# Performance work log

Measured on AMD Instinct MI355X. Metric: run time of the kernel, lower is better.

The kernel has to match this reference:

```python
import jax, jax.numpy as jnp
import numpy as np

N_SAMPLES = 256   # n_samples from __init__
N_THIN = 10       # N from __init__
N_WORDS = 4096


def setup_inputs() -> dict:
    key = jax.random.key(0)
    k1, k2, k3 = jax.random.split(key, 3)
    # scale potentials so per-step weight deltas stay in a sane exp() range
    bigram = jax.random.normal(k1, (N_WORDS, N_WORDS), dtype=jnp.float32)
    start = jax.random.normal(k2, (N_WORDS,), dtype=jnp.float32)
    end = jax.random.normal(k3, (N_WORDS,), dtype=jnp.float32)
    return {"n_words": N_WORDS, "bigram": bigram, "start": start, "end": end}


def _mh_chain(bigram, start, end, n_words, chain_size, rng):
    # chain[0] = identity permutation (random_start=False)
    perm0 = jnp.arange(n_words, dtype=jnp.int32)
    w0 = bigram[perm0[:-1], perm0[1:]].sum() + start[perm0[0]] + end[perm0[-1]]

    def step(carry, k):
        perm, w_last = carry
        k_pos, k_cat, k_u = jax.random.split(k, 3)
        # pick a token to move, remove it -> perm2 of length n_words-1
        pos = jax.random.randint(k_pos, (), 0, n_words)
        to_move = perm[pos]
        j = jnp.arange(n_words - 1)
        perm2 = perm[j + (j >= pos).astype(j.dtype)]
        # insertion logits over n_words slots (self._probs, unnormalized log p)
        logits = jnp.zeros((n_words,), dtype=bigram.dtype)
        logits = logits.at[0].add(start[to_move]).at[-1].add(end[to_move])
        logits = logits.at[1:].add(bigram[perm2, to_move])   # left-neighbor term
        logits = logits.at[:-1].add(bigram[to_move, perm2])  # right-neighbor term
        p = jax.nn.softmax(logits)
        new_pos = jax.random.categorical(k_cat, logits)
        # insert to_move at new_pos
        jj = jnp.arange(n_words)
        shifted = perm2[jnp.clip(jj - (jj > new_pos).astype(jj.dtype), 0, n_words - 2)]
        sample = jnp.where(jj == new_pos, to_move, shifted).astype(perm.dtype)
        # new chain weight
        new_w = bigram[sample[:-1], sample[1:]].sum() + start[sample[0]] + end[sample[-1]]
        # MH accept ratio; removing to_move from sample recovers perm2, so the
        # reverse insertion distribution equals p -> ratio p[new_pos]/p[pos]
        acc = jnp.minimum(1.0, jnp.exp(new_w - w_last) * p[new_pos] / p[pos])
        accept = acc > jax.random.uniform(k_u, ())
        perm_next = jnp.where(accept, sample, perm)
        w_next = jnp.where(accept, new_w, w_last)
        return (perm_next, w_next), perm_next

    keys = jax.random.split(rng, chain_size - 1)
    _, perms = jax.lax.scan(step, (perm0, w0), keys)
    chain = jnp.concatenate([perm0[None, :], perms], axis=0)  # [chain_size, n_words]
    sel = jnp.arange(0, chain_size, N_THIN) + (N_THIN - 1)    # thin: every N-th state
    return chain[sel]


def reference(n_words, bigram, start, end):
    chain_size = N_SAMPLES * N_THIN
    rng = jax.random.key(42)
    return _mh_chain(bigram, start, end, n_words, chain_size, rng)
```

## Files before the change

kernel.cpp:

```cpp
#include <hip/hip_runtime.h>
#include <stdint.h>


#define NW 4096
#define NSTEPS 2559
#define NTHREADS 1024
#define NWAVES 16

typedef unsigned long long u64;
typedef uint32_t u32;
typedef unsigned short u16;

__device__ __forceinline__ u32 rotl32(u32 v, u32 r) { return (v << r) | (v >> (32u - r)); }

__device__ __forceinline__ void tf2x32(u32 k0, u32 k1, u32 x0, u32 x1, u32* o0, u32* o1) {
  u32 ks2 = k0 ^ k1 ^ 0x1BD11BDAu;
  x0 += k0; x1 += k1;
#define TFR(r0, r1, r2, r3)                      \
  x0 += x1; x1 = rotl32(x1, r0); x1 ^= x0;       \
  x0 += x1; x1 = rotl32(x1, r1); x1 ^= x0;       \
  x0 += x1; x1 = rotl32(x1, r2); x1 ^= x0;       \
  x0 += x1; x1 = rotl32(x1, r3); x1 ^= x0;
  TFR(13, 15, 26, 6)  x0 += k1;  x1 += ks2 + 1u;
  TFR(17, 29, 16, 24) x0 += ks2; x1 += k0 + 2u;
  TFR(13, 15, 26, 6)  x0 += k0;  x1 += k1 + 3u;
  TFR(17, 29, 16, 24) x0 += k1;  x1 += ks2 + 4u;
  TFR(13, 15, 26, 6)  x0 += ks2; x1 += k0 + 5u;
#undef TFR
  *o0 = x0; *o1 = x1;
}

__device__ __forceinline__ float unif01(u32 bits) {
  return __uint_as_float((bits >> 9) | 0x3f800000u) - 1.0f;
}

__device__ __forceinline__ u32 fkey(float f) {
  u32 b = __float_as_uint(f);
  return b ^ ((b >> 31) ? 0xFFFFFFFFu : 0x80000000u);
}


template <int CTRL>
__device__ __forceinline__ u32 dpp32(u32 v) {
  return (u32)__builtin_amdgcn_update_dpp(0, (int)v, CTRL, 0xF, 0xF, true);
}

template <int CTRL>
__device__ __forceinline__ void dppmax64(u32& hi, u32& lo) {
  u32 h2 = dpp32<CTRL>(hi);
  u32 l2 = dpp32<CTRL>(lo);
  bool g = (h2 > hi) || (h2 == hi && l2 > lo);
  hi = g ? h2 : hi;
  lo = g ? l2 : lo;
}

__device__ __forceinline__ u64 wave_max_u64(u64 key) {
  u32 lo = (u32)key, hi = (u32)(key >> 32);
  dppmax64<0x111>(hi, lo); dppmax64<0x112>(hi, lo);
  dppmax64<0x114>(hi, lo); dppmax64<0x118>(hi, lo);
  dppmax64<0x142>(hi, lo); dppmax64<0x143>(hi, lo);
  return ((u64)hi << 32) | lo;
}

__device__ __forceinline__ u64 bfly16_max_u64(u64 key) {
  u32 lo = (u32)key, hi = (u32)(key >> 32);
  dppmax64<0xB1>(hi, lo); dppmax64<0x4E>(hi, lo);
  dppmax64<0x141>(hi, lo); dppmax64<0x140>(hi, lo);
  return ((u64)hi << 32) | lo;
}


#define TT 32
__global__ void transpose_k(const float* __restrict__ in, float* __restrict__ out) {
  __shared__ float tile[TT][TT + 1];
  int x = blockIdx.x * TT + threadIdx.x;
  int y = blockIdx.y * TT + threadIdx.y;
  for (int j = 0; j < TT; j += 8) tile[threadIdx.y + j][threadIdx.x] = in[(u64)(y + j) * NW + x];
  __syncthreads();
  x = blockIdx.y * TT + threadIdx.x;
  y = blockIdx.x * TT + threadIdx.y;
  for (int j = 0; j < TT; j += 8) out[(u64)(y + j) * NW + x] = tile[threadIdx.x][threadIdx.y + j];
}

__global__ void gumbel_k(float* __restrict__ gumb) {
  long long idx = (long long)blockIdx.x * blockDim.x + threadIdx.x;
  if (idx >= (long long)NSTEPS * NW) return;
  int t = (int)(idx >> 12);
  int p = (int)(idx & (NW - 1));
  int i = (p >> 2) | ((p & 3) << 10);
  u32 kt0, kt1, kc0, kc1, ba, bb;
  tf2x32(0u, 42u, 0u, (u32)t, &kt0, &kt1);
  tf2x32(kt0, kt1, 0u, 1u, &kc0, &kc1);
  tf2x32(kc0, kc1, 0u, (u32)i, &ba, &bb);
  float u = unif01(ba ^ bb);
  if (u == 0.0f) u = 1.17549435e-38f;
  float t1 = (float)log((double)u);
  float t2 = (float)log((double)(-t1));
  gumb[idx] = -t2;
}

__global__ void posu_k(int* __restrict__ posArr, float* __restrict__ uArr) {
  int t = blockIdx.x * blockDim.x + threadIdx.x;
  if (t >= NSTEPS) return;
  u32 kt0, kt1, kp0, kp1, ku0, ku1, k2a, k2b, ra, rb, ua, ub;
  tf2x32(0u, 42u, 0u, (u32)t, &kt0, &kt1);
  tf2x32(kt0, kt1, 0u, 0u, &kp0, &kp1);
  tf2x32(kt0, kt1, 0u, 2u, &ku0, &ku1);
  tf2x32(kp0, kp1, 0u, 1u, &k2a, &k2b);
  tf2x32(k2a, k2b, 0u, 0u, &ra, &rb);
  posArr[t] = (int)((ra ^ rb) & (u32)(NW - 1));
  tf2x32(ku0, ku1, 0u, 0u, &ua, &ub);
  uArr[t] = unif01(ua ^ ub);
}


#define SAMPLE_AT(idx)                                                        \
  ((idx) < np ? (int)s_perm[(idx) + ((idx) >= pos)]                           \
              : ((idx) == np ? tm                                             \
                             : (int)s_perm[((idx)-1) + (((idx)-1) >= pos)]))

__global__ __launch_bounds__(NTHREADS)
void mcmc_fast10(const float* __restrict__ bigram,
                 const float* __restrict__ bigT,
                 const float* __restrict__ gumb,
                 const int* __restrict__ posArr,
                 const float* __restrict__ uArr,
                 const float* __restrict__ startv,
                 const float* __restrict__ endv,
                 int* __restrict__ out) {
  __shared__ u16    s_perm[NW];
  __shared__ float  s_rowB[NW];
  __shared__ float  s_rowT[NW];
  __shared__ u64    s_redu[NWAVES];
  __shared__ float  s_stm, s_etm, s_lpos;
  __shared__ int    s_accs;

  const int tid = threadIdx.x;
  const int lane = tid & 63;
  const int wid = tid >> 6;

  for (int i = tid; i < NW; i += NTHREADS) s_perm[i] = (u16)i;

  int pos = posArr[0];
  int tm = pos;
  {
    float4 rb4 = ((const float4*)(bigram + (u64)tm * NW))[tid];
    float4 rt4 = ((const float4*)(bigT + (u64)tm * NW))[tid];
    ((float4*)s_rowB)[tid] = rb4;
    ((float4*)s_rowT)[tid] = rt4;
  }
  if (tid == 0) { s_stm = startv[tm]; s_etm = endv[tm]; }

  float u_cur = uArr[0];
  float start_cur = startv[0];
  float end_cur = endv[NW - 1];
  float brg = 0.0f;
  if (pos >= 1 && pos <= NW - 2) brg = bigram[(u64)(pos - 1) * NW + (pos + 1)];

  float4 g4 = ((const float4*)gumb)[tid];
  __syncthreads();

  for (int t = 0; t < NSTEPS; ++t) {
    const float gg[4] = {g4.x, g4.y, g4.z, g4.w};
    int pos_nxt; float u_nxt;
    {
      int tn = (t + 1 < NSTEPS) ? (t + 1) : (NSTEPS - 1);
      g4 = ((const float4*)(gumb + ((u64)tn << 12)))[tid];
      pos_nxt = posArr[tn];
      u_nxt = uArr[tn];
    }
    u64 best = 0;
#pragma unroll
    for (int k = 0; k < 4; ++k) {
      int i = tid + k * NTHREADS;
      float li;
      if (i == 0) {
        int r = s_perm[(0 >= pos) ? 1 : 0];
        li = s_stm + s_rowB[r];
      } else if (i == NW - 1) {
        int l = s_perm[((NW - 2) >= pos) ? (NW - 1) : (NW - 2)];
        li = s_etm + s_rowT[l];
      } else {
        int l = s_perm[(i - 1) + ((i - 1) >= pos)];
        int r = s_perm[i + (i >= pos)];
        li = s_rowT[l] + s_rowB[r];
      }
      if (i == pos) s_lpos = li;
      float sv = gg[k] + li;
      u64 key = ((u64)fkey(sv) << 32) | (u32)(NW - 1 - i);
      if (key > best) best = key;
    }
    best = wave_max_u64(best);
    if (lane == 63) s_redu[wid] = best;
    __syncthreads();

    int np;
    {
      u64 bb = bfly16_max_u64(s_redu[lane & 15]);
      np = NW - 1 - (int)(bb & 0xFFFFFFFFu);
    }
    const int tmR = (int)s_perm[pos_nxt];
    const int tmA = SAMPLE_AT(pos_nxt);
    u16 stash[4];
#pragma unroll
    for (int k = 0; k < 4; ++k) {
      int j = tid + k * NTHREADS;
      stash[k] = (j < np) ? s_perm[j + (j >= pos)]
                          : ((j == np) ? (u16)tm : s_perm[(j - 1) + ((j - 1) >= pos)]);
    }
    int plA = 0, prA = 0, plR = 0, prR = 0;
    const bool ibn = (pos_nxt >= 1 && pos_nxt <= NW - 2);
    if (wid == 0) {
      int ls_i = (np >= 1) ? ((np - 1) + ((np - 1) >= pos)) : 0;
      int rs_i = (np <= NW - 2) ? (np + (np >= pos)) : 0;
      const int l_s = (int)s_perm[ls_i];
      const int r_s = (int)s_perm[rs_i];
      float splitv = bigram[(u64)l_s * NW + r_s];
      int s0 = (np > 0) ? (int)s_perm[(0 >= pos) ? 1 : 0] : tm;
      int sl = (np < NW - 1) ? (int)s_perm[(NW - 2) + ((NW - 2) >= pos)] : tm;
      float sv0 = startv[s0];
      float ev1 = endv[sl];
      float remL = 0.0f, remR = 0.0f;
      if (pos > 0)      remL = s_rowT[s_perm[pos - 1]];
      if (pos < NW - 1) remR = s_rowB[s_perm[pos + 1]];
      float vnpm1 = (np >= 1)      ? s_rowT[l_s] : 0.0f;
      float vnp   = (np <= NW - 2) ? s_rowB[r_s] : 0.0f;
      if (ibn) {
        plR = (int)s_perm[pos_nxt - 1]; prR = (int)s_perm[pos_nxt + 1];
        plA = SAMPLE_AT(pos_nxt - 1);   prA = SAMPLE_AT(pos_nxt + 1);
      }
      float stm_r = s_stm, etm_r = s_etm;
      float lposv = s_lpos;
      double delta = 0.0;
      if (pos > 0)               delta -= (double)remL;
      if (pos < NW - 1)          delta -= (double)remR;
      if (pos > 0 && pos < NW-1) delta += (double)brg;
      if (np > 0)                delta += (double)vnpm1;
      if (np < NW - 1)           delta += (double)vnp;
      if (np > 0 && np < NW - 1) delta -= (double)splitv;
      delta += ((double)sv0 - (double)start_cur) + ((double)ev1 - (double)end_cur);
      float lnp = (np == 0) ? (stm_r + vnp)
                : ((np == NW - 1) ? (etm_r + vnpm1) : (vnpm1 + vnp));
      double ed = delta + ((double)lnp - (double)lposv);
      float a = fminf(1.0f, (float)exp(ed));
      int acc = (a > u_cur) ? 1 : 0;
      if (lane == 0) s_accs = acc;
      if (acc) { start_cur = sv0; end_cur = ev1; }
    }
    __syncthreads();

    const int acc = s_accs;
    const int tm_next = acc ? tmA : tmR;
    const float4 rb4 = ((const float4*)(bigram + (u64)tm_next * NW))[tid];
    const float4 rt4 = ((const float4*)(bigT + (u64)tm_next * NW))[tid];
    if (wid == 0) {
      float stmN = startv[tm_next];
      float etmN = endv[tm_next];
      brg = 0.0f;
      if (ibn) {
        int pl = acc ? plA : plR;
        int pr = acc ? prA : prR;
        brg = bigram[(u64)pl * NW + pr];
      }
      if (lane == 0) { s_stm = stmN; s_etm = etmN; }
    }
    if (acc) {
#pragma unroll
      for (int k = 0; k < 4; ++k) {
        int j = tid + k * NTHREADS;
        s_perm[j] = stash[k];
      }
    }
    ((float4*)s_rowB)[tid] = rb4;
    ((float4*)s_rowT)[tid] = rt4;
    tm = tm_next;
    pos = pos_nxt;
    u_cur = u_nxt;
    __syncthreads();

    if ((t % 10) == 8) {
      int row = (t - 8) / 10;
      ushort4 p4 = ((const ushort4*)s_perm)[tid];
      int4 o4;
      o4.x = (int)p4.x; o4.y = (int)p4.y; o4.z = (int)p4.z; o4.w = (int)p4.w;
      ((int4*)(out + (u64)row * NW))[tid] = o4;
    }
  }
}


__global__ __launch_bounds__(NTHREADS)
void mcmc_kernel(const float* __restrict__ bigram,
                 const float* __restrict__ startv,
                 const float* __restrict__ endv,
                 int* __restrict__ out) {
  __shared__ int    s_perm[NW];
  __shared__ float  s_logit[NW];
  __shared__ float  s_gath[NW];
  __shared__ float  s_redf[NWAVES];
  __shared__ u64    s_redu[NWAVES];
  __shared__ double s_redd[NWAVES];
  __shared__ float  s_m, s_Z, s_w;
  __shared__ int    s_pos, s_tm, s_np, s_acc;
  __shared__ u32    s_kcat0, s_kcat1, s_ku0, s_ku1;

  const int tid = threadIdx.x;
  const int lane = tid & 63;
  const int wid = tid >> 6;

  for (int i = tid; i < NW; i += NTHREADS) s_perm[i] = i;
  for (int j = tid; j < NW - 1; j += NTHREADS) s_gath[j] = bigram[(u64)j * NW + (j + 1)];
  __syncthreads();
  if (tid == 0) {
    float S = 0.0f;
    for (int j = 0; j < NW - 1; ++j) S += s_gath[j];
    S = S + startv[0];
    S = S + endv[NW - 1];
    s_w = S;
  }
  __syncthreads();

  for (int t = 0; t < NSTEPS; ++t) {
    if (tid == 0) {
      u32 kt0, kt1;
      tf2x32(0u, 42u, 0u, (u32)t, &kt0, &kt1);
      u32 kp0, kp1, kc0, kc1, ku0, ku1;
      tf2x32(kt0, kt1, 0u, 0u, &kp0, &kp1);
      tf2x32(kt0, kt1, 0u, 1u, &kc0, &kc1);
      tf2x32(kt0, kt1, 0u, 2u, &ku0, &ku1);
      u32 k2a, k2b, ra, rb;
      tf2x32(kp0, kp1, 0u, 1u, &k2a, &k2b);
      tf2x32(k2a, k2b, 0u, 0u, &ra, &rb);
      int pos = (int)((ra ^ rb) & (u32)(NW - 1));
      s_pos = pos;
      s_tm = s_perm[pos];
      s_kcat0 = kc0; s_kcat1 = kc1; s_ku0 = ku0; s_ku1 = ku1;
    }
    __syncthreads();
    const int pos = s_pos, tm = s_tm;

    float lmax = -3.402823466e+38f;
    for (int i = tid; i < NW; i += NTHREADS) {
      float li;
      if (i == 0) {
        int r = s_perm[(0 >= pos) ? 1 : 0];
        li = startv[tm] + bigram[(u64)tm * NW + r];
      } else if (i == NW - 1) {
        int l = s_perm[((NW - 2) >= pos) ? (NW - 1) : (NW - 2)];
        li = endv[tm] + bigram[(u64)l * NW + tm];
      } else {
        int l = s_perm[((i - 1) >= pos) ? i : (i - 1)];
        int r = s_perm[(i >= pos) ? (i + 1) : i];
        li = bigram[(u64)l * NW + tm] + bigram[(u64)tm * NW + r];
      }
      s_logit[i] = li;
      lmax = fmaxf(lmax, li);
    }
    for (int o = 32; o > 0; o >>= 1) lmax = fmaxf(lmax, __shfl_down(lmax, o, 64));
    if (lane == 0) s_redf[wid] = lmax;
    __syncthreads();
    if (tid == 0) {
      float m = s_redf[0];
      for (int w = 1; w < NWAVES; ++w) m = fmaxf(m, s_redf[w]);
      s_m = m;
    }
    __syncthreads();
    const float m = s_m;

    double zacc = 0.0;
    u64 best = 0;
    const u32 kc0 = s_kcat0, kc1 = s_kcat1;
    for (int i = tid; i < NW; i += NTHREADS) {
      float li = s_logit[i];
      float ex = (float)exp((double)(li - m));
      zacc += (double)ex;
      u32 ba, bb;
      tf2x32(kc0, kc1, 0u, (u32)i, &ba, &bb);
      float u = unif01(ba ^ bb);
      if (u == 0.0f) u = 1.17549435e-38f;
      float t1 = (float)log((double)u);
      float t2 = (float)log((double)(-t1));
      float g = -t2;
      float sv = g + li;
      u64 key = ((u64)fkey(sv) << 32) | (u32)(NW - 1 - i);
      if (key > best) best = key;
    }
    for (int o = 32; o > 0; o >>= 1) {
      u64 w = __shfl_down(best, o, 64);
      if (w > best) best = w;
      zacc += __shfl_down(zacc, o, 64);
    }
    if (lane == 0) { s_redu[wid] = best; s_redd[wid] = zacc; }
    __syncthreads();
    if (tid == 0) {
      u64 b = s_redu[0]; double z = s_redd[0];
      for (int w = 1; w < NWAVES; ++w) {
        if (s_redu[w] > b) b = s_redu[w];
        z += s_redd[w];
      }
      s_np = NW - 1 - (int)(b & 0xFFFFFFFFu);
      s_Z = (float)z;
    }
    __syncthreads();
    const int np = s_np;

    for (int j = tid; j < NW - 1; j += NTHREADS) {
      int a = (j < np) ? s_perm[j + (j >= pos)]
                       : ((j == np) ? tm : s_perm[(j - 1) + ((j - 1) >= pos)]);
      int j1 = j + 1;
      int b = (j1 < np) ? s_perm[j1 + (j1 >= pos)]
                        : ((j1 == np) ? tm : s_perm[(j1 - 1) + ((j1 - 1) >= pos)]);
      s_gath[j] = bigram[(u64)a * NW + b];
    }
    __syncthreads();

    if (tid == 0) {
      float S = 0.0f;
      for (int j = 0; j < NW - 1; ++j) S += s_gath[j];
      int s0 = (0 < np) ? s_perm[(0 >= pos) ? 1 : 0] : tm;
      int sl = ((NW - 1) == np) ? tm : s_perm[(NW - 2) + ((NW - 2) >= pos)];
      S = S + startv[s0];
      S = S + endv[sl];
      float dw = S - s_w;
      float e1 = (float)exp((double)dw);
      float en = (float)exp((double)(s_logit[np] - m));
      float eo = (float)exp((double)(s_logit[pos] - m));
      float pn = en / s_Z;
      float po = eo / s_Z;
      float acc = e1 * pn;
      acc = acc / po;
      acc = fminf(1.0f, acc);
      u32 ua, ub;
      tf2x32(s_ku0, s_ku1, 0u, 0u, &ua, &ub);
      float u = unif01(ua ^ ub);
      int accept = (acc > u) ? 1 : 0;
      s_acc = accept;
      if (accept) s_w = S;
    }
    __syncthreads();

    int stash[4];
    if (s_acc) {
      for (int k = 0; k < 4; ++k) {
        int i = tid + k * NTHREADS;
        stash[k] = (i < np) ? s_perm[i + (i >= pos)]
                            : ((i == np) ? tm : s_perm[(i - 1) + ((i - 1) >= pos)]);
      }
    }
    __syncthreads();
    if (s_acc) {
      for (int k = 0; k < 4; ++k) {
        int i = tid + k * NTHREADS;
        s_perm[i] = stash[k];
      }
    }
    __syncthreads();

    if (((t + 1) % 10) == 9) {
      int row = (t - 8) / 10;
      for (int i = tid; i < NW; i += NTHREADS) out[(u64)row * NW + i] = s_perm[i];
    }
    __syncthreads();
  }
}

extern "C" void kernel_launch(void* const* d_in, const int* in_sizes, int n_in,
                              void* d_out, int out_size, void* d_ws, size_t ws_size,
                              hipStream_t stream) {
  const float* bigram = (const float*)d_in[1];
  const float* startv = (const float*)d_in[2];
  const float* endv   = (const float*)d_in[3];
  int* out = (int*)d_out;

  const size_t needT = (size_t)NW * NW * sizeof(float);
  const size_t needG = (size_t)NSTEPS * NW * sizeof(float);
  const size_t needP = (size_t)NSTEPS * (sizeof(int) + sizeof(float));

  if (ws_size >= needT + needG + needP) {
    float* bigT = (float*)d_ws;
    float* gumb = (float*)((char*)d_ws + needT);
    int* posArr = (int*)((char*)d_ws + needT + needG);
    float* uArr = (float*)((char*)d_ws + needT + needG + (size_t)NSTEPS * sizeof(int));
    hipLaunchKernelGGL(transpose_k, dim3(NW / TT, NW / TT), dim3(TT, 8), 0, stream,
                       bigram, bigT);
    long long ng = (long long)NSTEPS * NW;
    hipLaunchKernelGGL(gumbel_k, dim3((unsigned)((ng + 255) / 256)), dim3(256), 0, stream,
                       gumb);
    hipLaunchKernelGGL(posu_k, dim3((NSTEPS + 255) / 256), dim3(256), 0, stream,
                       posArr, uArr);
    hipLaunchKernelGGL(mcmc_fast10, dim3(1), dim3(NTHREADS), 0, stream,
                       bigram, bigT, gumb, posArr, uArr, startv, endv, out);
  } else {
    hipLaunchKernelGGL(mcmc_kernel, dim3(1), dim3(NTHREADS), 0, stream,
                       bigram, startv, endv, out);
  }
}
```

Measured before the change: 7.521 ms.

## Interleave bigram rows in LDS and assign contiguous slots per thread with DPP neighbors

Each thread now owns four consecutive insertion slots instead of four strided ones. It reads its perm entries with a single ushort4 load and gets neighbouring entries via DPP lane shifts. The two per-step bigram rows are interleaved into a single float2 array so that left and right terms come from one LDS read, and the gumbel layout is changed to match. The accept exponential also switches from double exp to float expf. This cuts LDS traffic and index arithmetic in the serial per-step loop, but float2 gathers may add bank conflicts, and expf could shift the accept decision in rare borderline cases.

```diff
diff --git a/kernel.cpp b/kernel.cpp
--- a/kernel.cpp
+++ b/kernel.cpp
@@ -86,8 +86,7 @@
   long long idx = (long long)blockIdx.x * blockDim.x + threadIdx.x;
   if (idx >= (long long)NSTEPS * NW) return;
   int t = (int)(idx >> 12);
-  int p = (int)(idx & (NW - 1));
-  int i = (p >> 2) | ((p & 3) << 10);
+  int i = (int)(idx & (NW - 1));
   u32 kt0, kt1, kc0, kc1, ba, bb;
   tf2x32(0u, 42u, 0u, (u32)t, &kt0, &kt1);
   tf2x32(kt0, kt1, 0u, 1u, &kc0, &kc1);
@@ -120,7 +119,7 @@
                              : (int)s_perm[((idx)-1) + (((idx)-1) >= pos)]))
 
 __global__ __launch_bounds__(NTHREADS)
-void mcmc_fast10(const float* __restrict__ bigram,
+void mcmc_fast11(const float* __restrict__ bigram,
                  const float* __restrict__ bigT,
                  const float* __restrict__ gumb,
                  const int* __restrict__ posArr,
@@ -129,8 +128,7 @@
                  const float* __restrict__ endv,
                  int* __restrict__ out) {
   __shared__ u16    s_perm[NW];
-  __shared__ float  s_rowB[NW];
-  __shared__ float  s_rowT[NW];
+  __shared__ float2 s_rows[NW];
   __shared__ u64    s_redu[NWAVES];
   __shared__ float  s_stm, s_etm, s_lpos;
   __shared__ int    s_accs;
@@ -138,6 +136,7 @@
   const int tid = threadIdx.x;
   const int lane = tid & 63;
   const int wid = tid >> 6;
+  const int j0 = tid * 4;
 
   for (int i = tid; i < NW; i += NTHREADS) s_perm[i] = (u16)i;
 
@@ -146,8 +145,8 @@
   {
     float4 rb4 = ((const float4*)(bigram + (u64)tm * NW))[tid];
     float4 rt4 = ((const float4*)(bigT + (u64)tm * NW))[tid];
-    ((float4*)s_rowB)[tid] = rb4;
-    ((float4*)s_rowT)[tid] = rt4;
+    ((float4*)(&s_rows[j0]))[0] = make_float4(rt4.x, rb4.x, rt4.y, rb4.y);
+    ((float4*)(&s_rows[j0]))[1] = make_float4(rt4.z, rb4.z, rt4.w, rb4.w);
   }
   if (tid == 0) { s_stm = startv[tm]; s_etm = endv[tm]; }
 
@@ -169,26 +168,47 @@
       pos_nxt = posArr[tn];
       u_nxt = uArr[tn];
     }
-    u64 best = 0;
-#pragma unroll
-    for (int k = 0; k < 4; ++k) {
-      int i = tid + k * NTHREADS;
-      float li;
-      if (i == 0) {
-        int r = s_perm[(0 >= pos) ? 1 : 0];
-        li = s_stm + s_rowB[r];
-      } else if (i == NW - 1) {
-        int l = s_perm[((NW - 2) >= pos) ? (NW - 1) : (NW - 2)];
-        li = s_etm + s_rowT[l];
-      } else {
-        int l = s_perm[(i - 1) + ((i - 1) >= pos)];
-        int r = s_perm[i + (i >= pos)];
-        li = s_rowT[l] + s_rowB[r];
-      }
-      if (i == pos) s_lpos = li;
-      float sv = gg[k] + li;
-      u64 key = ((u64)fkey(sv) << 32) | (u32)(NW - 1 - i);
-      if (key > best) best = key;
+    ushort4 pq = ((const ushort4*)s_perm)[tid];
+    const int p0i = pq.x, p1i = pq.y, p2i = pq.z, p3i = pq.w;
+    int pm1, pp4;
+    {
+      u32 lo = (u32)pq.x | ((u32)pq.y << 16);
+      u32 hi = (u32)pq.z | ((u32)pq.w << 16);
+      pm1 = (int)(dpp32<0x138>(hi) >> 16);
+      pp4 = (int)(dpp32<0x130>(lo) & 0xFFFFu);
+      if (lane == 0)  pm1 = (tid > 0) ? (int)s_perm[j0 - 1] : 0;
+      if (lane == 63) pp4 = (tid < NTHREADS - 1) ? (int)s_perm[j0 + 4] : 0;
+    }
+    const int w0 = (j0     >= pos) ? p1i : p0i;
+    const int w1 = (j0 + 1 >= pos) ? p2i : p1i;
+    const int w2 = (j0 + 2 >= pos) ? p3i : p2i;
+    const int w3 = (j0 + 3 >= pos) ? pp4 : p3i;
+    const int wprev = ((j0 - 1) >= pos) ? p0i : pm1;
+    const float2 f0 = s_rows[w0];
+    const float2 f1 = s_rows[w1];
+    const float2 f2 = s_rows[w2];
+    const float2 f3 = s_rows[w3];
+    float tprev = __uint_as_float(dpp32<0x138>(__float_as_uint(f3.x)));
+    if (lane == 0 && tid > 0) tprev = s_rows[wprev].x;
+    float li0 = tprev + f0.y;
+    float li1 = f0.x + f1.y;
+    float li2 = f1.x + f2.y;
+    float li3 = f2.x + f3.y;
+    if (tid == 0)            li0 = s_stm + f0.y;
+    if (tid == NTHREADS - 1) li3 = s_etm + f2.x;
+    if ((pos >> 2) == tid) {
+      int k = pos & 3;
+      s_lpos = (k == 0) ? li0 : ((k == 1) ? li1 : ((k == 2) ? li2 : li3));
+    }
+    u64 best;
+    {
+      u64 b0 = ((u64)fkey(gg[0] + li0) << 32) | (u32)(NW - 1 - j0);
+      u64 b1 = ((u64)fkey(gg[1] + li1) << 32) | (u32)(NW - 2 - j0);
+      u64 b2 = ((u64)fkey(gg[2] + li2) << 32) | (u32)(NW - 3 - j0);
+      u64 b3 = ((u64)fkey(gg[3] + li3) << 32) | (u32)(NW - 4 - j0);
+      best = b0 > b1 ? b0 : b1;
+      u64 b23 = b2 > b3 ? b2 : b3;
+      if (b23 > best) best = b23;
     }
     best = wave_max_u64(best);
     if (lane == 63) s_redu[wid] = best;
@@ -201,13 +221,11 @@
     }
     const int tmR = (int)s_perm[pos_nxt];
     const int tmA = SAMPLE_AT(pos_nxt);
-    u16 stash[4];
-#pragma unroll
-    for (int k = 0; k < 4; ++k) {
-      int j = tid + k * NTHREADS;
-      stash[k] = (j < np) ? s_perm[j + (j >= pos)]
-                          : ((j == np) ? (u16)tm : s_perm[(j - 1) + ((j - 1) >= pos)]);
-    }
+    ushort4 st;
+    st.x = (j0     < np) ? (u16)w0 : ((j0     == np) ? (u16)tm : (u16)wprev);
+    st.y = (j0 + 1 < np) ? (u16)w1 : ((j0 + 1 == np) ? (u16)tm : (u16)w0);
+    st.z = (j0 + 2 < np) ? (u16)w2 : ((j0 + 2 == np) ? (u16)tm : (u16)w1);
+    st.w = (j0 + 3 < np) ? (u16)w3 : ((j0 + 3 == np) ? (u16)tm : (u16)w2);
     int plA = 0, prA = 0, plR = 0, prR = 0;
     const bool ibn = (pos_nxt >= 1 && pos_nxt <= NW - 2);
     if (wid == 0) {
@@ -221,10 +239,10 @@
       float sv0 = startv[s0];
       float ev1 = endv[sl];
       float remL = 0.0f, remR = 0.0f;
-      if (pos > 0)      remL = s_rowT[s_perm[pos - 1]];
-      if (pos < NW - 1) remR = s_rowB[s_perm[pos + 1]];
-      float vnpm1 = (np >= 1)      ? s_rowT[l_s] : 0.0f;
-      float vnp   = (np <= NW - 2) ? s_rowB[r_s] : 0.0f;
+      if (pos > 0)      remL = s_rows[s_perm[pos - 1]].x;
+      if (pos < NW - 1) remR = s_rows[s_perm[pos + 1]].y;
+      float vnpm1 = (np >= 1)      ? s_rows[l_s].x : 0.0f;
+      float vnp   = (np <= NW - 2) ? s_rows[r_s].y : 0.0f;
       if (ibn) {
         plR = (int)s_perm[pos_nxt - 1]; prR = (int)s_perm[pos_nxt + 1];
         plA = SAMPLE_AT(pos_nxt - 1);   prA = SAMPLE_AT(pos_nxt + 1);
@@ -232,17 +250,17 @@
       float stm_r = s_stm, etm_r = s_etm;
       float lposv = s_lpos;
       double delta = 0.0;
-      if (pos > 0)               delta -= (double)remL;
-      if (pos < NW - 1)          delta -= (double)remR;
-      if (pos > 0 && pos < NW-1) delta += (double)brg;
-      if (np > 0)                delta += (double)vnpm1;
-      if (np < NW - 1)           delta += (double)vnp;
-      if (np > 0 && np < NW - 1) delta -= (double)splitv;
+      if (pos > 0)                 delta -= (double)remL;
+      if (pos < NW - 1)            delta -= (double)remR;
+      if (pos > 0 && pos < NW - 1) delta += (double)brg;
+      if (np > 0)                  delta += (double)vnpm1;
+      if (np < NW - 1)             delta += (double)vnp;
+      if (np > 0 && np < NW - 1)   delta -= (double)splitv;
       delta += ((double)sv0 - (double)start_cur) + ((double)ev1 - (double)end_cur);
       float lnp = (np == 0) ? (stm_r + vnp)
                 : ((np == NW - 1) ? (etm_r + vnpm1) : (vnpm1 + vnp));
       double ed = delta + ((double)lnp - (double)lposv);
-      float a = fminf(1.0f, (float)exp(ed));
+      float a = fminf(1.0f, expf((float)ed));
       int acc = (a > u_cur) ? 1 : 0;
       if (lane == 0) s_accs = acc;
       if (acc) { start_cur = sv0; end_cur = ev1; }
@@ -264,15 +282,9 @@
       }
       if (lane == 0) { s_stm = stmN; s_etm = etmN; }
     }
-    if (acc) {
-#pragma unroll
-      for (int k = 0; k < 4; ++k) {
-        int j = tid + k * NTHREADS;
-        s_perm[j] = stash[k];
-      }
-    }
-    ((float4*)s_rowB)[tid] = rb4;
-    ((float4*)s_rowT)[tid] = rt4;
+    if (acc) ((ushort4*)s_perm)[tid] = st;
+    ((float4*)(&s_rows[j0]))[0] = make_float4(rt4.x, rb4.x, rt4.y, rb4.y);
+    ((float4*)(&s_rows[j0]))[1] = make_float4(rt4.z, rb4.z, rt4.w, rb4.w);
     tm = tm_next;
     pos = pos_nxt;
     u_cur = u_nxt;
@@ -488,7 +500,7 @@
                        gumb);
     hipLaunchKernelGGL(posu_k, dim3((NSTEPS + 255) / 256), dim3(256), 0, stream,
                        posArr, uArr);
-    hipLaunchKernelGGL(mcmc_fast10, dim3(1), dim3(NTHREADS), 0, stream,
+    hipLaunchKernelGGL(mcmc_fast11, dim3(1), dim3(NTHREADS), 0, stream,
                        bigram, bigT, gumb, posArr, uArr, startv, endv, out);
   } else {
     hipLaunchKernelGGL(mcmc_kernel, dim3(1), dim3(NTHREADS), 0, stream,
```

Result: faster. 6.689 ms (-11.1%).
